# Performance work log

Hardware: AMD Instinct MI355X
Metric: run time of the kernel (lower is better)

The kernel has to match this reference:

```python
import jax, jax.numpy as jnp
import numpy as np

B, N, K_NBR = 8, 4096, 16
H1, H3 = 512, 64
NS = 24  # covariance neighborhood size (hardcoded in encode)


def _local_cov(pc, ns):
    # Vectorized equivalent of the per-point sliding-window covariance loop.
    Bv, Nv, D = pc.shape
    half = ns // 2
    offs = jnp.arange(-half, half + 1)              # window size ns+1 = 25
    idx = jnp.arange(Nv)[:, None] + offs            # [N, 25]
    valid = (idx >= 0) & (idx < Nv)
    nb = pc[:, jnp.clip(idx, 0, Nv - 1), :]         # [B, N, 25, D]
    vm = valid[None, :, :, None].astype(pc.dtype)
    cnt = valid.sum(-1).astype(pc.dtype)[None, :, None]  # actual window counts
    mean = (nb * vm).sum(2) / cnt                   # [B, N, D]
    cen = (nb - mean[:, :, None, :]) * vm           # mask after centering
    cov = jnp.einsum('bnwd,bnwe->bnde', cen, cen) / (ns - 1)  # torch divides by ns-1
    return cov.reshape(Bv, Nv, D * D)


def _gcn(h, src, dst, w, b):
    # torch_geometric GCNConv: add self-loops, sym-normalize, aggregate at dst.
    Nt = h.shape[0]
    loop = jnp.arange(Nt, dtype=src.dtype)
    s = jnp.concatenate([src, loop])
    d = jnp.concatenate([dst, loop])
    deg = jax.ops.segment_sum(jnp.ones_like(d, h.dtype), d, num_segments=Nt)
    dinv = jnp.where(deg > 0, jax.lax.rsqrt(deg), 0.0)
    hw = h @ w
    msg = (dinv[s] * dinv[d])[:, None] * hw[s]
    return jax.ops.segment_sum(msg, d, num_segments=Nt) + b


def setup_inputs() -> dict:
    key = jax.random.key(0)
    ks = jax.random.split(key, 10)

    def lin(k, fi, fo):
        w = jax.random.normal(k, (fi, fo), jnp.float32) / np.float32(np.sqrt(fi))
        return w, jnp.zeros((fo,), jnp.float32)

    x = jax.random.normal(ks[0], (B, N, 3), jnp.float32)
    knn = jax.random.randint(ks[1], (2, B * N * K_NBR), 0, B * N, jnp.int32)
    w_e1, b_e1 = lin(ks[2], 12, H3)
    w_g1, b_g1 = lin(ks[3], H3, 2 * H3)
    w_g2, b_g2 = lin(ks[4], 2 * H3, H1)
    w_e2, b_e2 = lin(ks[5], H1, H1)
    w_d1, b_d1 = lin(ks[6], H1 + 2, 3)
    w_d2, b_d2 = lin(ks[7], H1 + 3, 3)
    return dict(x=x, knn=knn, w_e1=w_e1, b_e1=b_e1, w_g1=w_g1, b_g1=b_g1,
                w_g2=w_g2, b_g2=b_g2, w_e2=w_e2, b_e2=b_e2,
                w_d1=w_d1, b_d1=b_d1, w_d2=w_d2, b_d2=b_d2)


def reference(x, knn, w_e1, b_e1, w_g1, b_g1, w_g2, b_g2,
              w_e2, b_e2, w_d1, b_d1, w_d2, b_d2):
    act = jax.nn.selu
    Bv, Nv, _ = x.shape
    # ---- encode ----
    cov = _local_cov(x, NS)                                  # [B, N, 9]
    h = act(jnp.concatenate([x, cov], -1) @ w_e1 + b_e1)     # [B, N, H3]
    h = h.reshape(Bv * Nv, -1)
    h = act(_gcn(h, knn[0], knn[1], w_g1, b_g1))             # [B*N, 2*H3]
    h = act(_gcn(h, knn[0], knn[1], w_g2, b_g2))             # [B*N, H1]
    h = h.reshape(Bv, Nv, -1)
    lat = h.max(axis=1, keepdims=True)                       # AdaptiveMaxPool1d(1)
    lat = act(lat @ w_e2 + b_e2)                             # [B, 1, H1]
    # ---- decode ----
    nx = int(1 + (Nv * 120 / 60) ** 0.5)
    ny = int(1 + (Nv * 60 / 120) ** 0.5)
    xg = jnp.linspace(1.0, 120.0, nx)
    yg = jnp.linspace(1.0, 60.0, ny)
    grid = jnp.stack(jnp.meshgrid(xg, yg, indexing='ij'), -1).reshape(-1, 2)[:Nv]
    y = jnp.broadcast_to(grid[None], (Bv, Nv, 2))
    xr = jnp.broadcast_to(lat, (Bv, Nv, lat.shape[-1]))      # repeat codeword
    k = act(jnp.concatenate([xr, y], -1) @ w_d1 + b_d1)      # [B, N, 3]
    out = act(jnp.concatenate([xr, k], -1) @ w_d2 + b_d2)    # [B, N, 3]
    return out
```

## Files before the change

### kernel.cpp

```cpp
#include <hip/hip_runtime.h>
#include <math.h>

#define SELU_SCALE 1.0507009873554804934193349852946f
#define SELU_ALPHA 1.6732632423543772848170429916717f

typedef short bf16x8 __attribute__((ext_vector_type(8)));
typedef float f32x4 __attribute__((ext_vector_type(4)));

__device__ __forceinline__ float selu_f(float x) {
    return SELU_SCALE * (x > 0.f ? x : SELU_ALPHA * expm1f(x));
}

__device__ __forceinline__ unsigned short f2bf(float f) {
    unsigned int u = __float_as_uint(f);
    u += 0x7FFF + ((u >> 16) & 1);
    return (unsigned short)(u >> 16);
}
__device__ __forceinline__ float bflo(unsigned int u) { return __uint_as_float(u << 16); }
__device__ __forceinline__ float bfhi(unsigned int u) { return __uint_as_float(u & 0xFFFF0000u); }

__device__ __forceinline__ unsigned int fenc(float f) {
    unsigned int u = __float_as_uint(f);
    return (u & 0x80000000u) ? ~u : (u | 0x80000000u);
}
__device__ __forceinline__ float fdec(unsigned int u) {
    return __uint_as_float((u & 0x80000000u) ? (u ^ 0x80000000u) : ~u);
}

__device__ __forceinline__ void acc8(float* a, uint4 v) {
    a[0] += bflo(v.x); a[1] += bfhi(v.x);
    a[2] += bflo(v.y); a[3] += bfhi(v.y);
    a[4] += bflo(v.z); a[5] += bfhi(v.z);
    a[6] += bflo(v.w); a[7] += bfhi(v.w);
}

__device__ __forceinline__ uint4 pack8(const float* a, float dv) {
    uint4 pk;
    pk.x = (unsigned int)f2bf(a[0] * dv) | ((unsigned int)f2bf(a[1] * dv) << 16);
    pk.y = (unsigned int)f2bf(a[2] * dv) | ((unsigned int)f2bf(a[3] * dv) << 16);
    pk.z = (unsigned int)f2bf(a[4] * dv) | ((unsigned int)f2bf(a[5] * dv) << 16);
    pk.w = (unsigned int)f2bf(a[6] * dv) | ((unsigned int)f2bf(a[7] * dv) << 16);
    return pk;
}

__global__ __launch_bounds__(256) void prep_kernel(
    int* __restrict__ cnt, unsigned int* __restrict__ pad1,
    unsigned int* __restrict__ pad2, unsigned int* __restrict__ menc,
    const float* __restrict__ W1, unsigned short* __restrict__ Wp1,
    const float* __restrict__ W2, unsigned short* __restrict__ Wp2) {
    int b = blockIdx.x;
    int t = threadIdx.x;
    if (b < 128) {
        cnt[b * 256 + t] = 0;
    } else if (b == 128) {
        if (t < 32) pad1[t] = 0;
        if (t < 64) pad2[t] = 0;
        for (int i = t; i < 4096; i += 256) menc[i] = 0u;
    } else {
        if (t >= 64) return;
        int fb = b - 129;
        const float* W; unsigned short* Wp; int K, N, f;
        if (fb < 16) { W = W1; Wp = Wp1; K = 64; N = 128; f = fb; }
        else         { W = W2; Wp = Wp2; K = 128; N = 512; f = fb - 16; }
        int l = t;
        int KS = K / 32;
        int nt = f / KS, ks = f % KS;
        int ncol = nt * 16 + (l & 15);
        int k0 = ks * 32 + (l >> 4) * 8;
        unsigned short v[8];
        #pragma unroll
        for (int j = 0; j < 8; j++) v[j] = f2bf(W[(size_t)(k0 + j) * N + ncol]);
        *(uint4*)&Wp[((size_t)f * 64 + l) * 8] = *(uint4*)v;
    }
}

__global__ __launch_bounds__(256) void count_scatter_kernel(
    const int* __restrict__ src, const int* __restrict__ dst,
    int* __restrict__ cnt, int* __restrict__ ssrc, int E) {
    int e = blockIdx.x * 256 + threadIdx.x;
    if (e >= E) return;
    int d = dst[e];
    int pos = atomicAdd(&cnt[d], 1);
    if (pos < 64) ssrc[((size_t)d << 6) + pos] = src[e];
}

__global__ __launch_bounds__(256) void padfill_kernel(
    const int* __restrict__ cnt, float* __restrict__ dinv,
    int* __restrict__ pcnt, int* __restrict__ ssrc, int n) {
    int i = blockIdx.x * 256 + threadIdx.x;
    if (i >= n) return;
    int c = cnt[i];
    dinv[i] = rsqrtf((float)(c + 1));
    int pc = (c + 7) & ~7;
    if (pc > 64) pc = 64;
    pcnt[i] = pc;
    int* row = ssrc + ((size_t)i << 6);
    for (int k = c; k < pc; k++) row[k] = n;
}

__global__ __launch_bounds__(256) void cov_kernel(
    const float* __restrict__ x, const float* __restrict__ w_e1,
    const float* __restrict__ b_e1, const float* __restrict__ dinv,
    unsigned short* __restrict__ hs1) {
    __shared__ float Wl[12 * 64];
    __shared__ float Bl[64];
    __shared__ float xs[280 * 3];
    int t = threadIdx.x;
    int cb = blockIdx.x;
    for (int i = t; i < 768; i += 256) Wl[i] = w_e1[i];
    if (t < 64) Bl[t] = b_e1[t];
    int p0 = cb * 256;
    int n0 = p0 & 4095;
    const float* xb = x + (size_t)(p0 - n0) * 3;
    for (int idx = t; idx < 840; idx += 256) {
        int slot = idx / 3, d = idx - slot * 3;
        int g = n0 - 12 + slot;
        g = g < 0 ? 0 : (g > 4095 ? 4095 : g);
        xs[idx] = xb[g * 3 + d];
    }
    __syncthreads();
    int p = p0 + t;
    int n = n0 + t;
    int lo = n - 12 < 0 ? 0 : n - 12;
    int hi = n + 12 > 4095 ? 4095 : n + 12;
    int slo = lo - n0 + 12, shi = hi - n0 + 12;
    float sx = 0.f, sy = 0.f, sz = 0.f;
    float sxx = 0.f, sxy = 0.f, sxz = 0.f, syy = 0.f, syz = 0.f, szz = 0.f;
    for (int s = slo; s <= shi; s++) {
        float xv = xs[s * 3 + 0], yv = xs[s * 3 + 1], zv = xs[s * 3 + 2];
        sx += xv; sy += yv; sz += zv;
        sxx = fmaf(xv, xv, sxx); sxy = fmaf(xv, yv, sxy); sxz = fmaf(xv, zv, sxz);
        syy = fmaf(yv, yv, syy); syz = fmaf(yv, zv, syz); szz = fmaf(zv, zv, szz);
    }
    float cntf = (float)(shi - slo + 1);
    float rin = 1.f / cntf;
    float mx = sx * rin, my = sy * rin, mz = sz * rin;
    const float inv23 = 1.f / 23.f;
    float c00 = (sxx - sx * mx) * inv23;
    float c01 = (sxy - sx * my) * inv23;
    float c02 = (sxz - sx * mz) * inv23;
    float c11 = (syy - sy * my) * inv23;
    float c12 = (syz - sy * mz) * inv23;
    float c22 = (szz - sz * mz) * inv23;
    float feat[12];
    feat[0] = xs[(t + 12) * 3 + 0];
    feat[1] = xs[(t + 12) * 3 + 1];
    feat[2] = xs[(t + 12) * 3 + 2];
    feat[3] = c00; feat[4] = c01; feat[5]  = c02;
    feat[6] = c01; feat[7] = c11; feat[8]  = c12;
    feat[9] = c02; feat[10] = c12; feat[11] = c22;
    float dv = dinv[p];
    unsigned int* hp = (unsigned int*)(hs1 + (size_t)p * 64);
    for (int c = 0; c < 64; c += 2) {
        float a0 = Bl[c], a1 = Bl[c + 1];
        #pragma unroll
        for (int i = 0; i < 12; i++) {
            a0 = fmaf(feat[i], Wl[i * 64 + c], a0);
            a1 = fmaf(feat[i], Wl[i * 64 + c + 1], a1);
        }
        unsigned int pk = (unsigned int)f2bf(dv * selu_f(a0)) |
                          ((unsigned int)f2bf(dv * selu_f(a1)) << 16);
        hp[c >> 1] = pk;
    }
}

template <int C>
__global__ __launch_bounds__(256) void agg_kernel(
    const unsigned short* __restrict__ hs, const float* __restrict__ dinv,
    const int* __restrict__ pcnt, const int* __restrict__ ssrc,
    unsigned short* __restrict__ out, int n_nodes) {
    constexpr int TPN = C / 8;
    int node = blockIdx.x * (256 / TPN) + threadIdx.x / TPN;
    int cq = threadIdx.x % TPN;
    if (node >= n_nodes) return;
    const uint4* hp = (const uint4*)hs;
    float a[8];
    {
        uint4 u = hp[(size_t)node * TPN + cq];
        a[0] = bflo(u.x); a[1] = bfhi(u.x);
        a[2] = bflo(u.y); a[3] = bfhi(u.y);
        a[4] = bflo(u.z); a[5] = bfhi(u.z);
        a[6] = bflo(u.w); a[7] = bfhi(u.w);
    }
    int pc = pcnt[node];
    const int* sp = ssrc + ((size_t)node << 6);
    for (int j = 0; j < pc; j += 8) {
        int4 sa = *(const int4*)&sp[j];
        int4 sb = *(const int4*)&sp[j + 4];
        uint4 v0 = hp[(size_t)sa.x * TPN + cq];
        uint4 v1 = hp[(size_t)sa.y * TPN + cq];
        uint4 v2 = hp[(size_t)sa.z * TPN + cq];
        uint4 v3 = hp[(size_t)sa.w * TPN + cq];
        uint4 v4 = hp[(size_t)sb.x * TPN + cq];
        uint4 v5 = hp[(size_t)sb.y * TPN + cq];
        uint4 v6 = hp[(size_t)sb.z * TPN + cq];
        uint4 v7 = hp[(size_t)sb.w * TPN + cq];
        acc8(a, v0); acc8(a, v1); acc8(a, v2); acc8(a, v3);
        acc8(a, v4); acc8(a, v5); acc8(a, v6); acc8(a, v7);
    }
    ((uint4*)out)[(size_t)node * TPN + cq] = pack8(a, dinv[node]);
}

__global__ __launch_bounds__(256) void gemm1_kernel(
    const unsigned short* __restrict__ A, const unsigned short* __restrict__ Wp,
    const float* __restrict__ bias, const float* __restrict__ dinv,
    unsigned short* __restrict__ hs2) {
    constexpr int LDA = 72;
    __shared__ unsigned short As[128 * LDA];
    int t = threadIdx.x;
    int R0 = blockIdx.x * 128;

    for (int c = t; c < 128 * 8; c += 256) {
        int row = c >> 3, off = c & 7;
        *(uint4*)&As[row * LDA + off * 8] =
            *(const uint4*)&A[(size_t)(R0 + row) * 64 + off * 8];
    }
    __syncthreads();

    int wave = t >> 6, l = t & 63;
    int ml = l & 15, q = l >> 4;
    int wr = wave * 32;
    f32x4 acc[2][8];
    #pragma unroll
    for (int mf = 0; mf < 2; mf++)
        #pragma unroll
        for (int nf = 0; nf < 8; nf++) acc[mf][nf] = (f32x4){0.f, 0.f, 0.f, 0.f};
    const bf16x8* wp8 = (const bf16x8*)Wp;
    #pragma unroll
    for (int ks = 0; ks < 2; ks++) {
        bf16x8 af[2];
        #pragma unroll
        for (int mf = 0; mf < 2; mf++)
            af[mf] = *(const bf16x8*)&As[(wr + mf * 16 + ml) * LDA + ks * 32 + q * 8];
        bf16x8 bfr[8];
        #pragma unroll
        for (int nf = 0; nf < 8; nf++)
            bfr[nf] = wp8[(size_t)(nf * 2 + ks) * 64 + l];
        #pragma unroll
        for (int mf = 0; mf < 2; mf++)
            #pragma unroll
            for (int nf = 0; nf < 8; nf++)
                acc[mf][nf] = __builtin_amdgcn_mfma_f32_16x16x32_bf16(
                    af[mf], bfr[nf], acc[mf][nf], 0, 0, 0);
    }
    float bj[8];
    #pragma unroll
    for (int nf = 0; nf < 8; nf++) bj[nf] = bias[nf * 16 + ml];
    #pragma unroll
    for (int mf = 0; mf < 2; mf++) {
        #pragma unroll
        for (int r = 0; r < 4; r++) {
            int row = R0 + wr + mf * 16 + q * 4 + r;
            float dv = dinv[row];
            #pragma unroll
            for (int nf = 0; nf < 8; nf++) {
                float v = dv * selu_f(acc[mf][nf][r] + bj[nf]);
                hs2[(size_t)row * 128 + nf * 16 + ml] = f2bf(v);
            }
        }
    }
}

__global__ __launch_bounds__(256) void gemm2_kernel(
    const unsigned short* __restrict__ A, const unsigned short* __restrict__ Wp,
    const float* __restrict__ bias, unsigned int* __restrict__ menc, int Nfull) {
    constexpr int KS = 4;
    constexpr int LDA = 136;
    constexpr int CPR = 16;
    __shared__ unsigned short As[128 * LDA];
    int t = threadIdx.x;
    int wave = t >> 6, l = t & 63;
    int ml = l & 15, q = l >> 4;
    int R0 = blockIdx.x * 128;
    int cb = blockIdx.y * 128;

    for (int c = t; c < 128 * CPR; c += 256) {
        int row = c / CPR, off = c % CPR;
        *(uint4*)&As[row * LDA + off * 8] =
            *(const uint4*)&A[(size_t)(R0 + row) * 128 + off * 8];
    }
    __syncthreads();

    f32x4 acc[2][8];
    #pragma unroll
    for (int mf = 0; mf < 2; mf++)
        #pragma unroll
        for (int nf = 0; nf < 8; nf++) acc[mf][nf] = (f32x4){0.f, 0.f, 0.f, 0.f};

    const bf16x8* wp8 = (const bf16x8*)Wp;
    int wr = wave * 32;
    #pragma unroll
    for (int ks = 0; ks < KS; ks++) {
        bf16x8 af[2];
        #pragma unroll
        for (int mf = 0; mf < 2; mf++)
            af[mf] = *(const bf16x8*)&As[(wr + mf * 16 + ml) * LDA + ks * 32 + q * 8];
        bf16x8 bfr[8];
        #pragma unroll
        for (int nf = 0; nf < 8; nf++)
            bfr[nf] = wp8[(size_t)(((cb >> 4) + nf) * KS + ks) * 64 + l];
        #pragma unroll
        for (int mf = 0; mf < 2; mf++)
            #pragma unroll
            for (int nf = 0; nf < 8; nf++)
                acc[mf][nf] = __builtin_amdgcn_mfma_f32_16x16x32_bf16(
                    af[mf], bfr[nf], acc[mf][nf], 0, 0, 0);
    }

    float cmax[8];
    #pragma unroll
    for (int nf = 0; nf < 8; nf++) {
        float bj = bias[cb + nf * 16 + ml];
        float v = -INFINITY;
        #pragma unroll
        for (int mf = 0; mf < 2; mf++)
            #pragma unroll
            for (int r = 0; r < 4; r++)
                v = fmaxf(v, selu_f(acc[mf][nf][r] + bj));
        v = fmaxf(v, __shfl_xor(v, 16, 64));
        v = fmaxf(v, __shfl_xor(v, 32, 64));
        cmax[nf] = v;
    }
    __syncthreads();
    float* redf = (float*)As;
    if (ml == l) {
        #pragma unroll
        for (int nf = 0; nf < 8; nf++) redf[wave * 128 + nf * 16 + l] = cmax[nf];
    }
    __syncthreads();
    if (t < 128) {
        float v = redf[t];
        v = fmaxf(v, redf[128 + t]);
        v = fmaxf(v, redf[256 + t]);
        v = fmaxf(v, redf[384 + t]);
        int b = blockIdx.x >> 5;
        atomicMax(&menc[b * 512 + cb + t], fenc(v));
    }
}

__global__ __launch_bounds__(256) void lat_kernel(
    const unsigned int* __restrict__ menc, const float* __restrict__ w_e2,
    const float* __restrict__ b_e2, float* __restrict__ lat) {
    int b = blockIdx.x;
    int cg = blockIdx.y;
    int t = threadIdx.x;
    __shared__ float ml[512];
    __shared__ float red[8][32];
    ml[t] = fdec(menc[b * 512 + t]);
    ml[t + 256] = fdec(menc[b * 512 + t + 256]);
    __syncthreads();
    int cl = t & 31;
    int kg = t >> 5;
    int c = cg * 32 + cl;
    const float* wp = w_e2 + (size_t)(kg * 64) * 512 + c;
    const float* mlp = ml + kg * 64;
    float acc = 0.f;
    #pragma unroll 16
    for (int k = 0; k < 64; k++) acc = fmaf(mlp[k], wp[(size_t)k * 512], acc);
    red[kg][cl] = acc;
    __syncthreads();
    if (t < 32) {
        float v = ((red[0][t] + red[1][t]) + (red[2][t] + red[3][t])) +
                  ((red[4][t] + red[5][t]) + (red[6][t] + red[7][t]));
        lat[b * 512 + cg * 32 + t] = selu_f(v + b_e2[cg * 32 + t]);
    }
}

__global__ __launch_bounds__(256) void latw_decode_kernel(
    const float* __restrict__ lat, const float* __restrict__ w_d1,
    const float* __restrict__ b_d1, const float* __restrict__ w_d2,
    const float* __restrict__ b_d2, float* __restrict__ out) {
    int b = blockIdx.x >> 3;
    int sl = blockIdx.x & 7;
    int t = threadIdx.x;
    __shared__ float ll[512];
    __shared__ float red[6][256];
    __shared__ float lw[6];
    ll[t] = lat[b * 512 + t];
    ll[t + 256] = lat[b * 512 + t + 256];
    __syncthreads();
    float p[6] = {0.f, 0.f, 0.f, 0.f, 0.f, 0.f};
    for (int k = t; k < 512; k += 256) {
        float lv = ll[k];
        #pragma unroll
        for (int j = 0; j < 3; j++) {
            p[j]     = fmaf(lv, w_d1[k * 3 + j], p[j]);
            p[3 + j] = fmaf(lv, w_d2[k * 3 + j], p[3 + j]);
        }
    }
    #pragma unroll
    for (int j = 0; j < 6; j++) red[j][t] = p[j];
    __syncthreads();
    for (int s = 128; s > 0; s >>= 1) {
        if (t < s) {
            #pragma unroll
            for (int j = 0; j < 6; j++) red[j][t] += red[j][t + s];
        }
        __syncthreads();
    }
    if (t < 3) {
        lw[t]     = red[t][0] + b_d1[t];
        lw[3 + t] = red[3 + t][0] + b_d2[t];
    }
    __syncthreads();
    float l10 = lw[0], l11 = lw[1], l12 = lw[2];
    float l20 = lw[3], l21 = lw[4], l22 = lw[5];
    float w1a0 = w_d1[1536 + 0], w1a1 = w_d1[1536 + 1], w1a2 = w_d1[1536 + 2];
    float w1b0 = w_d1[1539 + 0], w1b1 = w_d1[1539 + 1], w1b2 = w_d1[1539 + 2];
    float w2a0 = w_d2[1536 + 0], w2a1 = w_d2[1536 + 1], w2a2 = w_d2[1536 + 2];
    float w2b0 = w_d2[1539 + 0], w2b1 = w_d2[1539 + 1], w2b2 = w_d2[1539 + 2];
    float w2c0 = w_d2[1542 + 0], w2c1 = w_d2[1542 + 1], w2c2 = w_d2[1542 + 2];
    {
        int n = sl * 512 + t;
        #pragma unroll
        for (int half = 0; half < 2; half++) {
            int i = n / 46;
            int j = n - i * 46;
            float y0 = fmaf((float)i, 119.f / 90.f, 1.f);
            float y1 = fmaf((float)j, 59.f / 45.f, 1.f);
            float k0 = selu_f(l10 + y0 * w1a0 + y1 * w1b0);
            float k1 = selu_f(l11 + y0 * w1a1 + y1 * w1b1);
            float k2 = selu_f(l12 + y0 * w1a2 + y1 * w1b2);
            float o0 = selu_f(l20 + k0 * w2a0 + k1 * w2b0 + k2 * w2c0);
            float o1 = selu_f(l21 + k0 * w2a1 + k1 * w2b1 + k2 * w2c1);
            float o2 = selu_f(l22 + k0 * w2a2 + k1 * w2b2 + k2 * w2c2);
            size_t pidx = (size_t)(b * 4096 + n) * 3;
            out[pidx + 0] = o0;
            out[pidx + 1] = o1;
            out[pidx + 2] = o2;
            n += 256;
        }
    }
}

extern "C" void kernel_launch(void* const* d_in, const int* in_sizes, int n_in,
                              void* d_out, int out_size, void* d_ws, size_t ws_size,
                              hipStream_t stream) {
    const float* x    = (const float*)d_in[0];
    const int*   knn  = (const int*)d_in[1];
    const float* w_e1 = (const float*)d_in[2];
    const float* b_e1 = (const float*)d_in[3];
    const float* w_g1 = (const float*)d_in[4];
    const float* b_g1 = (const float*)d_in[5];
    const float* w_g2 = (const float*)d_in[6];
    const float* b_g2 = (const float*)d_in[7];
    const float* w_e2 = (const float*)d_in[8];
    const float* b_e2 = (const float*)d_in[9];
    const float* w_d1 = (const float*)d_in[10];
    const float* b_d1 = (const float*)d_in[11];
    const float* w_d2 = (const float*)d_in[12];
    const float* b_d2 = (const float*)d_in[13];
    float* out = (float*)d_out;

    const int BN = in_sizes[0] / 3;
    const int E  = in_sizes[1] / 2;
    const int Bb = BN / 4096;
    const int* src = knn;
    const int* dst = knn + E;

    size_t off = 0;
    auto alloc = [&](size_t bytes) -> void* {
        void* p = (char*)d_ws + off;
        off += (bytes + 255) & ~(size_t)255;
        return p;
    };
    unsigned short* hs1 = (unsigned short*)alloc((size_t)(BN + 1) * 64 * 2);
    unsigned short* hs2 = (unsigned short*)alloc((size_t)(BN + 1) * 128 * 2);
    unsigned short* a1  = (unsigned short*)alloc((size_t)BN * 64 * 2);
    unsigned short* a2  = (unsigned short*)alloc((size_t)BN * 128 * 2);
    unsigned short* Wp1 = (unsigned short*)alloc((size_t)16 * 64 * 8 * 2);
    unsigned short* Wp2 = (unsigned short*)alloc((size_t)128 * 64 * 8 * 2);
    unsigned int* menc = (unsigned int*)alloc((size_t)Bb * 512 * 4);
    float* lat    = (float*)alloc((size_t)Bb * 512 * 4);
    float* dinv   = (float*)alloc((size_t)BN * 4);
    int*   cnt    = (int*)alloc((size_t)BN * 4);
    int*   pcnt   = (int*)alloc((size_t)BN * 4);
    int*   ssrc   = (int*)alloc((size_t)BN * 64 * 4);
    (void)ws_size;

    prep_kernel<<<273, 256, 0, stream>>>(
        cnt, (unsigned int*)(hs1 + (size_t)BN * 64),
        (unsigned int*)(hs2 + (size_t)BN * 128), menc, w_g1, Wp1, w_g2, Wp2);
    count_scatter_kernel<<<(E + 255) / 256, 256, 0, stream>>>(src, dst, cnt, ssrc, E);
    padfill_kernel<<<BN / 256, 256, 0, stream>>>(cnt, dinv, pcnt, ssrc, BN);
    cov_kernel<<<128, 256, 0, stream>>>(x, w_e1, b_e1, dinv, hs1);

    agg_kernel<64><<<BN / 32, 256, 0, stream>>>(hs1, dinv, pcnt, ssrc, a1, BN);
    gemm1_kernel<<<BN / 128, 256, 0, stream>>>(a1, Wp1, b_g1, dinv, hs2);

    agg_kernel<128><<<BN / 16, 256, 0, stream>>>(hs2, dinv, pcnt, ssrc, a2, BN);
    gemm2_kernel<<<dim3(BN / 128, 4), 256, 0, stream>>>(a2, Wp2, b_g2, menc, 512);

    lat_kernel<<<dim3(Bb, 16), 256, 0, stream>>>(menc, w_e2, b_e2, lat);

    latw_decode_kernel<<<Bb * 8, 256, 0, stream>>>(lat, w_d1, b_d1, w_d2, b_d2, out);
}
```

Measured before the change: 201.1 us.

## Fuse padfill with cov, and GCN aggregation with following GEMMs

Merges the padding/degree kernel into the covariance-encoder kernel, and fuses each GCN neighbor aggregation into its subsequent MFMA GEMM so aggregated rows go straight to shared memory instead of round-tripping through global buffers a1/a2. This removes three kernel launches and the intermediate writes and reads. gemm2 now loops over all four 128-column blocks within one block of 64 rows instead of splitting columns across the grid. The trade-off is fewer, larger blocks with less column parallelism and a gather phase that can stall the MFMA phase.

```diff
diff --git a/kernel.cpp b/kernel.cpp
--- a/kernel.cpp
+++ b/kernel.cpp
@@ -84,45 +84,43 @@
     if (pos < 64) ssrc[((size_t)d << 6) + pos] = src[e];
 }
 
-__global__ __launch_bounds__(256) void padfill_kernel(
+__global__ __launch_bounds__(128) void padfill_cov_kernel(
     const int* __restrict__ cnt, float* __restrict__ dinv,
-    int* __restrict__ pcnt, int* __restrict__ ssrc, int n) {
-    int i = blockIdx.x * 256 + threadIdx.x;
-    if (i >= n) return;
-    int c = cnt[i];
-    dinv[i] = rsqrtf((float)(c + 1));
+    int* __restrict__ pcnt, int* __restrict__ ssrc, int n,
+    const float* __restrict__ x, const float* __restrict__ w_e1,
+    const float* __restrict__ b_e1, unsigned short* __restrict__ hs1) {
+    __shared__ float Wl[12 * 64];
+    __shared__ float Bl[64];
+    __shared__ float xs[152 * 3];
+    int t = threadIdx.x;
+    int p0 = blockIdx.x * 128;
+    int p = p0 + t;
+
+    int c = cnt[p];
+    float dv = rsqrtf((float)(c + 1));
+    dinv[p] = dv;
     int pc = (c + 7) & ~7;
     if (pc > 64) pc = 64;
-    pcnt[i] = pc;
-    int* row = ssrc + ((size_t)i << 6);
-    for (int k = c; k < pc; k++) row[k] = n;
-}
-
-__global__ __launch_bounds__(256) void cov_kernel(
-    const float* __restrict__ x, const float* __restrict__ w_e1,
-    const float* __restrict__ b_e1, const float* __restrict__ dinv,
-    unsigned short* __restrict__ hs1) {
-    __shared__ float Wl[12 * 64];
-    __shared__ float Bl[64];
-    __shared__ float xs[280 * 3];
-    int t = threadIdx.x;
-    int cb = blockIdx.x;
-    for (int i = t; i < 768; i += 256) Wl[i] = w_e1[i];
+    pcnt[p] = pc;
+    {
+        int* row = ssrc + ((size_t)p << 6);
+        for (int k = c; k < pc; k++) row[k] = n;
+    }
+
+    for (int i = t; i < 768; i += 128) Wl[i] = w_e1[i];
     if (t < 64) Bl[t] = b_e1[t];
-    int p0 = cb * 256;
     int n0 = p0 & 4095;
     const float* xb = x + (size_t)(p0 - n0) * 3;
-    for (int idx = t; idx < 840; idx += 256) {
+    for (int idx = t; idx < 456; idx += 128) {
         int slot = idx / 3, d = idx - slot * 3;
         int g = n0 - 12 + slot;
         g = g < 0 ? 0 : (g > 4095 ? 4095 : g);
         xs[idx] = xb[g * 3 + d];
     }
     __syncthreads();
-    int p = p0 + t;
-    int n = n0 + t;
-    int lo = n - 12 < 0 ? 0 : n - 12;
-    int hi = n + 12 > 4095 ? 4095 : n + 12;
+    int nn = n0 + t;
+    int lo = nn - 12 < 0 ? 0 : nn - 12;
+    int hi = nn + 12 > 4095 ? 4095 : nn + 12;
     int slo = lo - n0 + 12, shi = hi - n0 + 12;
     float sx = 0.f, sy = 0.f, sz = 0.f;
     float sxx = 0.f, sxy = 0.f, sxz = 0.f, syy = 0.f, syz = 0.f, szz = 0.f;
@@ -149,192 +147,190 @@
     feat[3] = c00; feat[4] = c01; feat[5]  = c02;
     feat[6] = c01; feat[7] = c11; feat[8]  = c12;
     feat[9] = c02; feat[10] = c12; feat[11] = c22;
-    float dv = dinv[p];
     unsigned int* hp = (unsigned int*)(hs1 + (size_t)p * 64);
-    for (int c = 0; c < 64; c += 2) {
-        float a0 = Bl[c], a1 = Bl[c + 1];
+    for (int cc = 0; cc < 64; cc += 2) {
+        float a0 = Bl[cc], a1 = Bl[cc + 1];
         #pragma unroll
         for (int i = 0; i < 12; i++) {
-            a0 = fmaf(feat[i], Wl[i * 64 + c], a0);
-            a1 = fmaf(feat[i], Wl[i * 64 + c + 1], a1);
+            a0 = fmaf(feat[i], Wl[i * 64 + cc], a0);
+            a1 = fmaf(feat[i], Wl[i * 64 + cc + 1], a1);
         }
         unsigned int pk = (unsigned int)f2bf(dv * selu_f(a0)) |
                           ((unsigned int)f2bf(dv * selu_f(a1)) << 16);
-        hp[c >> 1] = pk;
-    }
-}
-
-template <int C>
-__global__ __launch_bounds__(256) void agg_kernel(
+        hp[cc >> 1] = pk;
+    }
+}
+
+__global__ __launch_bounds__(256) void agg_gemm1_kernel(
     const unsigned short* __restrict__ hs, const float* __restrict__ dinv,
     const int* __restrict__ pcnt, const int* __restrict__ ssrc,
-    unsigned short* __restrict__ out, int n_nodes) {
-    constexpr int TPN = C / 8;
-    int node = blockIdx.x * (256 / TPN) + threadIdx.x / TPN;
-    int cq = threadIdx.x % TPN;
-    if (node >= n_nodes) return;
-    const uint4* hp = (const uint4*)hs;
-    float a[8];
-    {
-        uint4 u = hp[(size_t)node * TPN + cq];
-        a[0] = bflo(u.x); a[1] = bfhi(u.x);
-        a[2] = bflo(u.y); a[3] = bfhi(u.y);
-        a[4] = bflo(u.z); a[5] = bfhi(u.z);
-        a[6] = bflo(u.w); a[7] = bfhi(u.w);
-    }
-    int pc = pcnt[node];
-    const int* sp = ssrc + ((size_t)node << 6);
-    for (int j = 0; j < pc; j += 8) {
-        int4 sa = *(const int4*)&sp[j];
-        int4 sb = *(const int4*)&sp[j + 4];
-        uint4 v0 = hp[(size_t)sa.x * TPN + cq];
-        uint4 v1 = hp[(size_t)sa.y * TPN + cq];
-        uint4 v2 = hp[(size_t)sa.z * TPN + cq];
-        uint4 v3 = hp[(size_t)sa.w * TPN + cq];
-        uint4 v4 = hp[(size_t)sb.x * TPN + cq];
-        uint4 v5 = hp[(size_t)sb.y * TPN + cq];
-        uint4 v6 = hp[(size_t)sb.z * TPN + cq];
-        uint4 v7 = hp[(size_t)sb.w * TPN + cq];
-        acc8(a, v0); acc8(a, v1); acc8(a, v2); acc8(a, v3);
-        acc8(a, v4); acc8(a, v5); acc8(a, v6); acc8(a, v7);
-    }
-    ((uint4*)out)[(size_t)node * TPN + cq] = pack8(a, dinv[node]);
-}
-
-__global__ __launch_bounds__(256) void gemm1_kernel(
-    const unsigned short* __restrict__ A, const unsigned short* __restrict__ Wp,
-    const float* __restrict__ bias, const float* __restrict__ dinv,
+    const unsigned short* __restrict__ Wp, const float* __restrict__ bias,
     unsigned short* __restrict__ hs2) {
     constexpr int LDA = 72;
-    __shared__ unsigned short As[128 * LDA];
-    int t = threadIdx.x;
-    int R0 = blockIdx.x * 128;
-
-    for (int c = t; c < 128 * 8; c += 256) {
-        int row = c >> 3, off = c & 7;
-        *(uint4*)&As[row * LDA + off * 8] =
-            *(const uint4*)&A[(size_t)(R0 + row) * 64 + off * 8];
+    __shared__ unsigned short As[64 * LDA];
+    int t = threadIdx.x;
+    int R0 = blockIdx.x * 64;
+    const uint4* hp = (const uint4*)hs;
+
+    #pragma unroll
+    for (int pass = 0; pass < 2; pass++) {
+        int rloc = pass * 32 + (t >> 3);
+        int node = R0 + rloc;
+        int cq = t & 7;
+        float a[8];
+        {
+            uint4 u = hp[(size_t)node * 8 + cq];
+            a[0] = bflo(u.x); a[1] = bfhi(u.x);
+            a[2] = bflo(u.y); a[3] = bfhi(u.y);
+            a[4] = bflo(u.z); a[5] = bfhi(u.z);
+            a[6] = bflo(u.w); a[7] = bfhi(u.w);
+        }
+        int pc = pcnt[node];
+        const int* sp = ssrc + ((size_t)node << 6);
+        for (int j = 0; j < pc; j += 8) {
+            int4 sa = *(const int4*)&sp[j];
+            int4 sb = *(const int4*)&sp[j + 4];
+            uint4 v0 = hp[(size_t)sa.x * 8 + cq];
+            uint4 v1 = hp[(size_t)sa.y * 8 + cq];
+            uint4 v2 = hp[(size_t)sa.z * 8 + cq];
+            uint4 v3 = hp[(size_t)sa.w * 8 + cq];
+            uint4 v4 = hp[(size_t)sb.x * 8 + cq];
+            uint4 v5 = hp[(size_t)sb.y * 8 + cq];
+            uint4 v6 = hp[(size_t)sb.z * 8 + cq];
+            uint4 v7 = hp[(size_t)sb.w * 8 + cq];
+            acc8(a, v0); acc8(a, v1); acc8(a, v2); acc8(a, v3);
+            acc8(a, v4); acc8(a, v5); acc8(a, v6); acc8(a, v7);
+        }
+        *(uint4*)&As[rloc * LDA + cq * 8] = pack8(a, dinv[node]);
     }
     __syncthreads();
 
     int wave = t >> 6, l = t & 63;
     int ml = l & 15, q = l >> 4;
-    int wr = wave * 32;
-    f32x4 acc[2][8];
-    #pragma unroll
-    for (int mf = 0; mf < 2; mf++)
-        #pragma unroll
-        for (int nf = 0; nf < 8; nf++) acc[mf][nf] = (f32x4){0.f, 0.f, 0.f, 0.f};
+    int wr = wave * 16;
+    f32x4 acc[8];
+    #pragma unroll
+    for (int nf = 0; nf < 8; nf++) acc[nf] = (f32x4){0.f, 0.f, 0.f, 0.f};
     const bf16x8* wp8 = (const bf16x8*)Wp;
     #pragma unroll
     for (int ks = 0; ks < 2; ks++) {
-        bf16x8 af[2];
-        #pragma unroll
-        for (int mf = 0; mf < 2; mf++)
-            af[mf] = *(const bf16x8*)&As[(wr + mf * 16 + ml) * LDA + ks * 32 + q * 8];
+        bf16x8 af = *(const bf16x8*)&As[(wr + ml) * LDA + ks * 32 + q * 8];
         bf16x8 bfr[8];
         #pragma unroll
         for (int nf = 0; nf < 8; nf++)
             bfr[nf] = wp8[(size_t)(nf * 2 + ks) * 64 + l];
         #pragma unroll
-        for (int mf = 0; mf < 2; mf++)
+        for (int nf = 0; nf < 8; nf++)
+            acc[nf] = __builtin_amdgcn_mfma_f32_16x16x32_bf16(
+                af, bfr[nf], acc[nf], 0, 0, 0);
+    }
+    float bj[8];
+    #pragma unroll
+    for (int nf = 0; nf < 8; nf++) bj[nf] = bias[nf * 16 + ml];
+    #pragma unroll
+    for (int r = 0; r < 4; r++) {
+        int row = R0 + wr + q * 4 + r;
+        float dv = dinv[row];
+        #pragma unroll
+        for (int nf = 0; nf < 8; nf++) {
+            float v = dv * selu_f(acc[nf][r] + bj[nf]);
+            hs2[(size_t)row * 128 + nf * 16 + ml] = f2bf(v);
+        }
+    }
+}
+
+__global__ __launch_bounds__(256) void agg_gemm2_kernel(
+    const unsigned short* __restrict__ hs, const float* __restrict__ dinv,
+    const int* __restrict__ pcnt, const int* __restrict__ ssrc,
+    const unsigned short* __restrict__ Wp, const float* __restrict__ bias,
+    unsigned int* __restrict__ menc) {
+    constexpr int KS = 4;
+    constexpr int LDA = 136;
+    __shared__ unsigned short As[64 * LDA];
+    __shared__ float redf[4 * 128];
+    int t = threadIdx.x;
+    int R0 = blockIdx.x * 64;
+    const uint4* hp = (const uint4*)hs;
+
+    #pragma unroll
+    for (int pass = 0; pass < 4; pass++) {
+        int rloc = pass * 16 + (t >> 4);
+        int node = R0 + rloc;
+        int cq = t & 15;
+        float a[8];
+        {
+            uint4 u = hp[(size_t)node * 16 + cq];
+            a[0] = bflo(u.x); a[1] = bfhi(u.x);
+            a[2] = bflo(u.y); a[3] = bfhi(u.y);
+            a[4] = bflo(u.z); a[5] = bfhi(u.z);
+            a[6] = bflo(u.w); a[7] = bfhi(u.w);
+        }
+        int pc = pcnt[node];
+        const int* sp = ssrc + ((size_t)node << 6);
+        for (int j = 0; j < pc; j += 8) {
+            int4 sa = *(const int4*)&sp[j];
+            int4 sb = *(const int4*)&sp[j + 4];
+            uint4 v0 = hp[(size_t)sa.x * 16 + cq];
+            uint4 v1 = hp[(size_t)sa.y * 16 + cq];
+            uint4 v2 = hp[(size_t)sa.z * 16 + cq];
+            uint4 v3 = hp[(size_t)sa.w * 16 + cq];
+            uint4 v4 = hp[(size_t)sb.x * 16 + cq];
+            uint4 v5 = hp[(size_t)sb.y * 16 + cq];
+            uint4 v6 = hp[(size_t)sb.z * 16 + cq];
+            uint4 v7 = hp[(size_t)sb.w * 16 + cq];
+            acc8(a, v0); acc8(a, v1); acc8(a, v2); acc8(a, v3);
+            acc8(a, v4); acc8(a, v5); acc8(a, v6); acc8(a, v7);
+        }
+        *(uint4*)&As[rloc * LDA + cq * 8] = pack8(a, dinv[node]);
+    }
+    __syncthreads();
+
+    int wave = t >> 6, l = t & 63;
+    int ml = l & 15, q = l >> 4;
+    int wr = wave * 16;
+    int b = blockIdx.x >> 6;
+    const bf16x8* wp8 = (const bf16x8*)Wp;
+    for (int cbi = 0; cbi < 4; cbi++) {
+        f32x4 acc[8];
+        #pragma unroll
+        for (int nf = 0; nf < 8; nf++) acc[nf] = (f32x4){0.f, 0.f, 0.f, 0.f};
+        #pragma unroll
+        for (int ks = 0; ks < KS; ks++) {
+            bf16x8 af = *(const bf16x8*)&As[(wr + ml) * LDA + ks * 32 + q * 8];
+            bf16x8 bfr[8];
             #pragma unroll
             for (int nf = 0; nf < 8; nf++)
-                acc[mf][nf] = __builtin_amdgcn_mfma_f32_16x16x32_bf16(
-                    af[mf], bfr[nf], acc[mf][nf], 0, 0, 0);
-    }
-    float bj[8];
-    #pragma unroll
-    for (int nf = 0; nf < 8; nf++) bj[nf] = bias[nf * 16 + ml];
-    #pragma unroll
-    for (int mf = 0; mf < 2; mf++) {
-        #pragma unroll
-        for (int r = 0; r < 4; r++) {
-            int row = R0 + wr + mf * 16 + q * 4 + r;
-            float dv = dinv[row];
-            #pragma unroll
-            for (int nf = 0; nf < 8; nf++) {
-                float v = dv * selu_f(acc[mf][nf][r] + bj[nf]);
-                hs2[(size_t)row * 128 + nf * 16 + ml] = f2bf(v);
-            }
-        }
-    }
-}
-
-__global__ __launch_bounds__(256) void gemm2_kernel(
-    const unsigned short* __restrict__ A, const unsigned short* __restrict__ Wp,
-    const float* __restrict__ bias, unsigned int* __restrict__ menc, int Nfull) {
-    constexpr int KS = 4;
-    constexpr int LDA = 136;
-    constexpr int CPR = 16;
-    __shared__ unsigned short As[128 * LDA];
-    int t = threadIdx.x;
-    int wave = t >> 6, l = t & 63;
-    int ml = l & 15, q = l >> 4;
-    int R0 = blockIdx.x * 128;
-    int cb = blockIdx.y * 128;
-
-    for (int c = t; c < 128 * CPR; c += 256) {
-        int row = c / CPR, off = c % CPR;
-        *(uint4*)&As[row * LDA + off * 8] =
-            *(const uint4*)&A[(size_t)(R0 + row) * 128 + off * 8];
-    }
-    __syncthreads();
-
-    f32x4 acc[2][8];
-    #pragma unroll
-    for (int mf = 0; mf < 2; mf++)
-        #pragma unroll
-        for (int nf = 0; nf < 8; nf++) acc[mf][nf] = (f32x4){0.f, 0.f, 0.f, 0.f};
-
-    const bf16x8* wp8 = (const bf16x8*)Wp;
-    int wr = wave * 32;
-    #pragma unroll
-    for (int ks = 0; ks < KS; ks++) {
-        bf16x8 af[2];
-        #pragma unroll
-        for (int mf = 0; mf < 2; mf++)
-            af[mf] = *(const bf16x8*)&As[(wr + mf * 16 + ml) * LDA + ks * 32 + q * 8];
-        bf16x8 bfr[8];
-        #pragma unroll
-        for (int nf = 0; nf < 8; nf++)
-            bfr[nf] = wp8[(size_t)(((cb >> 4) + nf) * KS + ks) * 64 + l];
-        #pragma unroll
-        for (int mf = 0; mf < 2; mf++)
+                bfr[nf] = wp8[(size_t)((cbi * 8 + nf) * KS + ks) * 64 + l];
             #pragma unroll
             for (int nf = 0; nf < 8; nf++)
-                acc[mf][nf] = __builtin_amdgcn_mfma_f32_16x16x32_bf16(
-                    af[mf], bfr[nf], acc[mf][nf], 0, 0, 0);
-    }
-
-    float cmax[8];
-    #pragma unroll
-    for (int nf = 0; nf < 8; nf++) {
-        float bj = bias[cb + nf * 16 + ml];
-        float v = -INFINITY;
-        #pragma unroll
-        for (int mf = 0; mf < 2; mf++)
+                acc[nf] = __builtin_amdgcn_mfma_f32_16x16x32_bf16(
+                    af, bfr[nf], acc[nf], 0, 0, 0);
+        }
+        float cmax[8];
+        #pragma unroll
+        for (int nf = 0; nf < 8; nf++) {
+            float bj = bias[cbi * 128 + nf * 16 + ml];
+            float v = -INFINITY;
             #pragma unroll
             for (int r = 0; r < 4; r++)
-                v = fmaxf(v, selu_f(acc[mf][nf][r] + bj));
-        v = fmaxf(v, __shfl_xor(v, 16, 64));
-        v = fmaxf(v, __shfl_xor(v, 32, 64));
-        cmax[nf] = v;
-    }
-    __syncthreads();
-    float* redf = (float*)As;
-    if (ml == l) {
-        #pragma unroll
-        for (int nf = 0; nf < 8; nf++) redf[wave * 128 + nf * 16 + l] = cmax[nf];
-    }
-    __syncthreads();
-    if (t < 128) {
-        float v = redf[t];
-        v = fmaxf(v, redf[128 + t]);
-        v = fmaxf(v, redf[256 + t]);
-        v = fmaxf(v, redf[384 + t]);
-        int b = blockIdx.x >> 5;
-        atomicMax(&menc[b * 512 + cb + t], fenc(v));
+                v = fmaxf(v, selu_f(acc[nf][r] + bj));
+            v = fmaxf(v, __shfl_xor(v, 16, 64));
+            v = fmaxf(v, __shfl_xor(v, 32, 64));
+            cmax[nf] = v;
+        }
+        __syncthreads();
+        if (ml == l) {
+            #pragma unroll
+            for (int nf = 0; nf < 8; nf++) redf[wave * 128 + nf * 16 + l] = cmax[nf];
+        }
+        __syncthreads();
+        if (t < 128) {
+            float v = redf[t];
+            v = fmaxf(v, redf[128 + t]);
+            v = fmaxf(v, redf[256 + t]);
+            v = fmaxf(v, redf[384 + t]);
+            atomicMax(&menc[b * 512 + cbi * 128 + t], fenc(v));
+        }
     }
 }
 
@@ -466,8 +462,6 @@
     };
     unsigned short* hs1 = (unsigned short*)alloc((size_t)(BN + 1) * 64 * 2);
     unsigned short* hs2 = (unsigned short*)alloc((size_t)(BN + 1) * 128 * 2);
-    unsigned short* a1  = (unsigned short*)alloc((size_t)BN * 64 * 2);
-    unsigned short* a2  = (unsigned short*)alloc((size_t)BN * 128 * 2);
     unsigned short* Wp1 = (unsigned short*)alloc((size_t)16 * 64 * 8 * 2);
     unsigned short* Wp2 = (unsigned short*)alloc((size_t)128 * 64 * 8 * 2);
     unsigned int* menc = (unsigned int*)alloc((size_t)Bb * 512 * 4);
@@ -482,14 +476,12 @@
         cnt, (unsigned int*)(hs1 + (size_t)BN * 64),
         (unsigned int*)(hs2 + (size_t)BN * 128), menc, w_g1, Wp1, w_g2, Wp2);
     count_scatter_kernel<<<(E + 255) / 256, 256, 0, stream>>>(src, dst, cnt, ssrc, E);
-    padfill_kernel<<<BN / 256, 256, 0, stream>>>(cnt, dinv, pcnt, ssrc, BN);
-    cov_kernel<<<128, 256, 0, stream>>>(x, w_e1, b_e1, dinv, hs1);
-
-    agg_kernel<64><<<BN / 32, 256, 0, stream>>>(hs1, dinv, pcnt, ssrc, a1, BN);
-    gemm1_kernel<<<BN / 128, 256, 0, stream>>>(a1, Wp1, b_g1, dinv, hs2);
-
-    agg_kernel<128><<<BN / 16, 256, 0, stream>>>(hs2, dinv, pcnt, ssrc, a2, BN);
-    gemm2_kernel<<<dim3(BN / 128, 4), 256, 0, stream>>>(a2, Wp2, b_g2, menc, 512);
+    padfill_cov_kernel<<<BN / 128, 128, 0, stream>>>(
+        cnt, dinv, pcnt, ssrc, BN, x, w_e1, b_e1, hs1);
+
+    agg_gemm1_kernel<<<BN / 64, 256, 0, stream>>>(hs1, dinv, pcnt, ssrc, Wp1, b_g1, hs2);
+
+    agg_gemm2_kernel<<<BN / 64, 256, 0, stream>>>(hs2, dinv, pcnt, ssrc, Wp2, b_g2, menc);
 
     lat_kernel<<<dim3(Bb, 16), 256, 0, stream>>>(menc, w_e2, b_e2, lat);
 
```

Measured after the change: 198.2 us. About the same (-1.4%).
